# Optimization experiments

Hardware: AMD Instinct MI355X
Metric: run time of the kernel (lower is better)

The kernel has to match this reference:

```python
import jax, jax.numpy as jnp
import numpy as np

S, B, D = 2048, 2, 1024
NH, DH, DI = 16, 64, 4096


def setup_inputs() -> dict:
    key = jax.random.key(0)
    ks = jax.random.split(key, 12)
    init_qkv = 1.0 / np.sqrt(D)
    init_out = 1.0 / np.sqrt(NH * DH)
    stdm = 1.0 / np.sqrt(D)
    stdi = 1.0 / np.sqrt(DI)

    def u(k, shape, lo, hi):
        return jax.random.uniform(k, shape, jnp.float32, lo, hi)

    inp = {}
    inp["dec_inp"] = jax.random.normal(ks[0], (S, B, D), jnp.float32)
    # causal mask: True = masked (future key j > query i); shape [q, k, batch]
    causal = jnp.triu(jnp.ones((S, S), bool), k=1)
    inp["attn_mask"] = jnp.broadcast_to(causal[:, :, None], (S, S, B))
    inp["query_mean"] = u(ks[1], (NH * DH, D), -init_qkv, init_qkv)
    inp["key_mean"] = u(ks[2], (NH * DH, D), -init_qkv, init_qkv)
    inp["value_mean"] = u(ks[3], (NH * DH, D), -init_qkv, init_qkv)
    inp["query_std"] = u(ks[4], (NH * DH, D), 2 * np.log(init_qkv), np.log(init_qkv))
    inp["key_std"] = u(ks[5], (NH * DH, D), 2 * np.log(init_qkv), np.log(init_qkv))
    inp["value_std"] = u(ks[6], (NH * DH, D), 2 * np.log(init_qkv), np.log(init_qkv))
    inp["output_mean"] = u(ks[7], (D, NH * DH), -init_out, init_out)
    inp["output_std"] = u(ks[8], (D, NH * DH), 2 * np.log(init_out), np.log(init_out))
    inp["ln1_gamma"] = jnp.ones((D,), jnp.float32)
    inp["ln1_beta"] = jnp.zeros((D,), jnp.float32)
    inp["w1_mean"] = u(ks[9], (DI, D), -stdm, stdm)
    inp["w2_mean"] = u(ks[10], (D, DI), -stdi, stdi)
    inp["w1_std"] = u(ks[11], (DI, D), 2 * np.log(stdm), np.log(stdm))
    inp["w2_std"] = u(jax.random.fold_in(key, 99), (D, DI), 2 * np.log(stdi), np.log(stdi))
    inp["ln2_gamma"] = jnp.ones((D,), jnp.float32)
    inp["ln2_beta"] = jnp.zeros((D,), jnp.float32)
    return inp


def _layer_norm(x, g, b, eps=1e-5):
    mu = jnp.mean(x, -1, keepdims=True)
    var = jnp.mean((x - mu) ** 2, -1, keepdims=True)
    return g * (x - mu) * jax.lax.rsqrt(var + eps) + b


def _kl(theta_mean, theta_std):
    return jnp.mean(theta_mean ** 2 - 2.0 * theta_std + jnp.exp(2.0 * theta_std)) / 2.0


def reference(dec_inp, attn_mask, query_mean, key_mean, value_mean, query_std,
              key_std, value_std, output_mean, output_std, ln1_gamma, ln1_beta,
              w1_mean, w2_mean, w1_std, w2_std, ln2_gamma, ln2_beta):
    scale = 1.0 / (DH ** 0.5)
    # QKV projections (eval mode: no Bayesian weight sampling, diffs are 0)
    head_q = jnp.einsum('ibd,hd->ibh', dec_inp, query_mean).reshape(S, B, NH, DH)
    head_k = jnp.einsum('ibd,hd->ibh', dec_inp, key_mean).reshape(S, B, NH, DH)
    head_v = jnp.einsum('ibd,hd->ibh', dec_inp, value_mean).reshape(S, B, NH, DH)
    attn_score = jnp.einsum('ibnd,jbnd->ijbn', head_q, head_k) * scale
    attn_score = jnp.where(attn_mask[:, :, :, None], -jnp.inf, attn_score)
    attn_prob = jax.nn.softmax(attn_score, axis=1)  # softmax over key dim j
    attn_vec = jnp.einsum('ijbn,jbnd->ibnd', attn_prob, head_v).reshape(S, B, NH * DH)
    # NOTE: the original code (bug-faithfully) projects with value_mean, not output_mean
    attn_out = jnp.einsum('ibh,dh->ibd', attn_vec, value_mean)
    h = _layer_norm(dec_inp + attn_out, ln1_gamma, ln1_beta)
    attn_kl = _kl(
        jnp.concatenate([query_mean, key_mean, value_mean, output_mean.T], -1),
        jnp.concatenate([query_std, key_std, value_std, output_std.T], -1))
    # Bayesian positionwise FF (no activation in BayesPositionwiseFF)
    l1 = jnp.einsum('ibd,fd->ibf', h, w1_mean)
    l2 = jnp.einsum('ibf,df->ibd', l1, w2_mean)
    out = _layer_norm(h + l2, ln2_gamma, ln2_beta)
    ff_kl = _kl(jnp.concatenate([w1_mean, w2_mean.T], -1),
                jnp.concatenate([w1_std, w2_std.T], -1))
    return out, attn_kl + ff_kl
```

## Files before the change

kernel.cpp:

```cpp
#include <hip/hip_runtime.h>

#define S_LEN  2048
#define BATCH  2
#define DMODEL 1024
#define NHEADS 16
#define DHEAD  64
#define DFF    4096
#define MROWS  (S_LEN*BATCH)
#define QKVN   3072

typedef __attribute__((ext_vector_type(8))) short bf16x8;
typedef __attribute__((ext_vector_type(4))) float f32x4;
typedef __attribute__((ext_vector_type(4))) short s16x4;

#define NEG_BIG (-3.0e38f)
#define SCALE_LOG2 (0.125f * 1.4426950408889634f)

__device__ __forceinline__ short f2bf(float f){
  unsigned u = __float_as_uint(f);
  u += 0x7fffu + ((u >> 16) & 1u);
  return (short)(u >> 16);
}

__device__ __forceinline__ void gload16(const void* gptr, void* lptr){
  __builtin_amdgcn_global_load_lds(
      (const __attribute__((address_space(1))) unsigned int*)gptr,
      (__attribute__((address_space(3))) unsigned int*)lptr,
      16, 0, 0);
}

__global__ __launch_bounds__(256) void cast_kernel(const float* __restrict__ in,
                                                   short* __restrict__ out, int n){
  int i = (blockIdx.x * 256 + threadIdx.x) * 4;
  if (i >= n) return;
  f32x4 v = *(const f32x4*)(in + i);
  s16x4 o;
  o[0] = f2bf(v[0]); o[1] = f2bf(v[1]); o[2] = f2bf(v[2]); o[3] = f2bf(v[3]);
  *(s16x4*)(out + i) = o;
}

__global__ __launch_bounds__(256) void cast_kl_kernel(const float* __restrict__ mean,
                                                      const float* __restrict__ stdv,
                                                      short* __restrict__ outb,
                                                      int n, double* acc){
  __shared__ double red[4];
  double local = 0.0;
  const int stride = gridDim.x * 1024;
  for (int i = (blockIdx.x * 256 + threadIdx.x) * 4; i < n; i += stride){
    f32x4 m = *(const f32x4*)(mean + i);
    f32x4 sv = *(const f32x4*)(stdv + i);
    if (outb){
      s16x4 o;
      o[0] = f2bf(m[0]); o[1] = f2bf(m[1]); o[2] = f2bf(m[2]); o[3] = f2bf(m[3]);
      *(s16x4*)(outb + i) = o;
    }
    for (int e = 0; e < 4; e++)
      local += (double)(m[e] * m[e]) - 2.0 * (double)sv[e] + (double)expf(2.f * sv[e]);
  }
  for (int msk = 1; msk < 64; msk <<= 1) local += __shfl_xor(local, msk, 64);
  const int t = threadIdx.x;
  if ((t & 63) == 0) red[t >> 6] = local;
  __syncthreads();
  if (t == 0) atomicAdd(acc, red[0] + red[1] + red[2] + red[3]);
}

__global__ void kl_final(const double* acc, float* out){
  out[0] = (float)(acc[0] / 8388608.0 + acc[1] / 16777216.0);
}

template<int BN>
__global__ __launch_bounds__(512) void gemm_bt(const short* __restrict__ A,
                                               const short* __restrict__ Bt,
                                               float* __restrict__ Cf,
                                               short* __restrict__ Cb,
                                               int M, int N, int K, int nbx){
  __shared__ short As[2][128][32];
  __shared__ short Bs[2][BN][32];
  constexpr int NB = BN / 32;
  const int t = threadIdx.x;
  const int lane = t & 63, w = t >> 6;
  const int q8 = (int)gridDim.x >> 3;
  const int sid = ((int)blockIdx.x & 7) * q8 + ((int)blockIdx.x >> 3);
  const int bx = sid % nbx, by = sid / nbx;
  const int m0 = by * 128, n0 = bx * BN;
  const int wm = (w & 3) * 32, wn = (w >> 2) * (BN / 2);
  const int lr = lane & 15, lg = lane >> 4;

  f32x4 acc[2][NB] = {};

  const short* Ap = A  + (size_t)(m0 + (t >> 2)) * K + (t & 3) * 8;
  const short* Bp = Bt + (size_t)(n0 + ((t & (BN * 4 - 1)) >> 2)) * K + (t & 3) * 8;
  char* ldsA0 = (char*)As + w * 1024;
  char* ldsB0 = (char*)Bs + (w & (NB * 2 - 1)) * 1024;
  constexpr int BSTRIDE = BN * 64;

  gload16(Ap, ldsA0);
  if (BN == 128 || t < 256) gload16(Bp, ldsB0);
  asm volatile("s_waitcnt vmcnt(0)" ::: "memory");
  __builtin_amdgcn_s_barrier();
  asm volatile("" ::: "memory");

  int cur = 0;
  for (int k0 = 0; k0 < K; k0 += 32){
    if (k0 + 32 < K){
      gload16(Ap + k0 + 32, ldsA0 + (cur ^ 1) * 8192);
      if (BN == 128 || t < 256) gload16(Bp + k0 + 32, ldsB0 + (cur ^ 1) * BSTRIDE);
    }
    bf16x8 a0 = *(const bf16x8*)&As[cur][wm      + lr][lg * 8];
    bf16x8 a1 = *(const bf16x8*)&As[cur][wm + 16 + lr][lg * 8];
    bf16x8 bfr[NB];
    for (int ni = 0; ni < NB; ni++)
      bfr[ni] = *(const bf16x8*)&Bs[cur][wn + ni * 16 + lr][lg * 8];
    for (int ni = 0; ni < NB; ni++){
      acc[0][ni] = __builtin_amdgcn_mfma_f32_16x16x32_bf16(a0, bfr[ni], acc[0][ni], 0, 0, 0);
      acc[1][ni] = __builtin_amdgcn_mfma_f32_16x16x32_bf16(a1, bfr[ni], acc[1][ni], 0, 0, 0);
    }
    asm volatile("s_waitcnt vmcnt(0)" ::: "memory");
    __builtin_amdgcn_s_barrier();
    asm volatile("" ::: "memory");
    cur ^= 1;
  }

  for (int mi = 0; mi < 2; mi++){
    for (int ni = 0; ni < NB; ni++){
      int row = m0 + wm + mi * 16 + lg * 4;
      int col = n0 + wn + ni * 16 + lr;
      for (int r = 0; r < 4; r++){
        float v = acc[mi][ni][r];
        if (Cf) Cf[(size_t)(row + r) * N + col] = v;
        if (Cb) Cb[(size_t)(row + r) * N + col] = f2bf(v);
      }
    }
  }
}

__global__ __launch_bounds__(256) void attn_kernel(const short* __restrict__ QKV,
                                                   short* __restrict__ AV){
  __shared__ short Ks[64][64];
  __shared__ short Vst[64][64];
  __shared__ short Pt[4][16][64];
  const int t = threadIdx.x, lane = t & 63, w = t >> 6;
  const int hb = blockIdx.y;
  const int b = hb >> 4, n = hb & 15;
  const int lr = lane & 15, lg = lane >> 4;

  for (int half = 0; half < 2; half++){
    const int qt = half ? (31 - (int)blockIdx.x) : (int)blockIdx.x;
    const int q0w = qt * 64 + w * 16;

    bf16x8 aq[2];
    {
      const short* qp = QKV + ((size_t)(q0w + lr) * BATCH + b) * QKVN + n * DHEAD + lg * 8;
      aq[0] = *(const bf16x8*)(qp);
      aq[1] = *(const bf16x8*)(qp + 32);
    }

    f32x4 acc[4] = {};
    float m_run = NEG_BIG, l_run = 0.f;

    for (int jt = 0; jt <= qt; jt++){
      const int j0 = jt * 64;
      __syncthreads();
      {
        int j = t >> 2, u0 = (t & 3) * 2;
        const short* kp = QKV + ((size_t)(j0 + j) * BATCH + b) * QKVN + DMODEL + n * DHEAD + u0 * 8;
        *(bf16x8*)&Ks[j][(u0 ^ (j & 7)) * 8]       = *(const bf16x8*)(kp);
        *(bf16x8*)&Ks[j][((u0 + 1) ^ (j & 7)) * 8] = *(const bf16x8*)(kp + 8);
        int jv = t & 63, dq = (t >> 6) * 16;
        const short* vp = QKV + ((size_t)(j0 + jv) * BATCH + b) * QKVN + 2 * DMODEL + n * DHEAD + dq;
        bf16x8 v0 = *(const bf16x8*)(vp);
        bf16x8 v1 = *(const bf16x8*)(vp + 8);
        int uj = jv >> 3, jl = jv & 7;
        for (int e = 0; e < 8; e++){
          int sc = (((uj ^ e) << 3) | jl);
          Vst[dq + e][sc]     = v0[e];
          Vst[dq + 8 + e][sc] = v1[e];
        }
      }
      __syncthreads();

      f32x4 s[4];
      __builtin_amdgcn_s_setprio(1);
      for (int nf = 0; nf < 4; nf++){
        f32x4 z = {};
        for (int kk = 0; kk < 2; kk++){
          bf16x8 bk = *(const bf16x8*)&Ks[nf * 16 + lr][((kk * 4 + lg) ^ (lr & 7)) * 8];
          z = __builtin_amdgcn_mfma_f32_16x16x32_bf16(bk, aq[kk], z, 0, 0, 0);
        }
        s[nf] = z;
      }
      __builtin_amdgcn_s_setprio(0);

      for (int nf = 0; nf < 4; nf++)
        for (int r = 0; r < 4; r++) s[nf][r] *= SCALE_LOG2;

      if (jt == qt){
        int qg = q0w + lr;
        for (int nf = 0; nf < 4; nf++)
          for (int r = 0; r < 4; r++)
            if (j0 + nf * 16 + lg * 4 + r > qg) s[nf][r] = NEG_BIG;
      }

      float mx = NEG_BIG;
      for (int nf = 0; nf < 4; nf++){
        float a0 = fmaxf(s[nf][0], s[nf][1]);
        float a1 = fmaxf(s[nf][2], s[nf][3]);
        mx = fmaxf(mx, fmaxf(a0, a1));
      }
      mx = fmaxf(mx, __shfl_xor(mx, 16, 64));
      mx = fmaxf(mx, __shfl_xor(mx, 32, 64));
      float mn = fmaxf(m_run, mx);
      float corr = __builtin_exp2f(m_run - mn);
      m_run = mn;

      float rs = 0.f;
      for (int nf = 0; nf < 4; nf++)
        for (int r = 0; r < 4; r++){
          float p = __builtin_exp2f(s[nf][r] - mn);
          s[nf][r] = p;
          rs += p;
        }
      rs += __shfl_xor(rs, 16, 64);
      rs += __shfl_xor(rs, 32, 64);
      l_run = l_run * corr + rs;

      char* prow = (char*)&Pt[w][lr][0];
      for (int nf = 0; nf < 4; nf++){
        unsigned u0 = __float_as_uint(s[nf][0]);
        unsigned u1 = __float_as_uint(s[nf][1]);
        unsigned u2 = __float_as_uint(s[nf][2]);
        unsigned u3 = __float_as_uint(s[nf][3]);
        uint2 val;
        val.x = (u0 >> 16) | (u1 & 0xffff0000u);
        val.y = (u2 >> 16) | (u3 & 0xffff0000u);
        int off = ((((nf * 2) + (lg >> 1)) ^ (lr & 7)) << 4) + ((lg & 1) << 3);
        *(uint2*)(prow + off) = val;
      }

      float cb[4];
      for (int r = 0; r < 4; r++) cb[r] = __shfl(corr, lg * 4 + r, 64);
      for (int df = 0; df < 4; df++)
        for (int r = 0; r < 4; r++) acc[df][r] *= cb[r];

      __builtin_amdgcn_s_setprio(1);
      for (int kk = 0; kk < 2; kk++){
        bf16x8 pa = *(const bf16x8*)(prow + ((((kk * 4) + lg) ^ (lr & 7)) << 4));
        for (int df = 0; df < 4; df++){
          bf16x8 bv = *(const bf16x8*)&Vst[df * 16 + lr][((kk * 4 + lg) ^ (lr & 7)) * 8];
          acc[df] = __builtin_amdgcn_mfma_f32_16x16x32_bf16(pa, bv, acc[df], 0, 0, 0);
        }
      }
      __builtin_amdgcn_s_setprio(0);
    }

    float lb[4];
    for (int r = 0; r < 4; r++) lb[r] = __shfl(l_run, lg * 4 + r, 64);
    for (int df = 0; df < 4; df++){
      for (int r = 0; r < 4; r++){
        int i_glob = q0w + lg * 4 + r;
        AV[((size_t)i_glob * BATCH + b) * DMODEL + n * DHEAD + df * 16 + lr] =
            f2bf(acc[df][r] / lb[r]);
      }
    }
    __syncthreads();
  }
}

__global__ __launch_bounds__(256) void ln_kernel(const float* __restrict__ xa,
                                                 const float* __restrict__ xb,
                                                 const float* __restrict__ gamma,
                                                 const float* __restrict__ beta,
                                                 float* __restrict__ outF,
                                                 short* __restrict__ outB){
  __shared__ float red[4];
  const int row = blockIdx.x, t = threadIdx.x;
  const size_t base = (size_t)row * DMODEL + t * 4;
  f32x4 a  = *(const f32x4*)(xa + base);
  f32x4 bb = *(const f32x4*)(xb + base);
  f32x4 x;
  for (int e = 0; e < 4; e++) x[e] = a[e] + bb[e];
  float sum = x[0] + x[1] + x[2] + x[3];
  for (int m = 1; m < 64; m <<= 1) sum += __shfl_xor(sum, m, 64);
  if ((t & 63) == 0) red[t >> 6] = sum;
  __syncthreads();
  float mu = (red[0] + red[1] + red[2] + red[3]) * (1.f / DMODEL);
  float sq = 0.f;
  for (int e = 0; e < 4; e++){ float d = x[e] - mu; sq += d * d; }
  for (int m = 1; m < 64; m <<= 1) sq += __shfl_xor(sq, m, 64);
  __syncthreads();
  if ((t & 63) == 0) red[t >> 6] = sq;
  __syncthreads();
  float var = (red[0] + red[1] + red[2] + red[3]) * (1.f / DMODEL);
  float rstd = rsqrtf(var + 1e-5f);
  f32x4 g  = *(const f32x4*)(gamma + t * 4);
  f32x4 be = *(const f32x4*)(beta + t * 4);
  for (int e = 0; e < 4; e++){
    float y = g[e] * (x[e] - mu) * rstd + be[e];
    if (outF) outF[base + e] = y;
    if (outB) outB[base + e] = f2bf(y);
  }
}

extern "C" void kernel_launch(void* const* d_in, const int* in_sizes, int n_in,
                              void* d_out, int out_size, void* d_ws, size_t ws_size,
                              hipStream_t stream){
  (void)in_sizes; (void)n_in; (void)out_size; (void)ws_size;
  const float* dec = (const float*)d_in[0];
  const float* qm  = (const float*)d_in[2];
  const float* km  = (const float*)d_in[3];
  const float* vm  = (const float*)d_in[4];
  const float* qs  = (const float*)d_in[5];
  const float* ks  = (const float*)d_in[6];
  const float* vs  = (const float*)d_in[7];
  const float* om  = (const float*)d_in[8];
  const float* os_ = (const float*)d_in[9];
  const float* g1  = (const float*)d_in[10];
  const float* b1  = (const float*)d_in[11];
  const float* w1m = (const float*)d_in[12];
  const float* w2m = (const float*)d_in[13];
  const float* w1s = (const float*)d_in[14];
  const float* w2s = (const float*)d_in[15];
  const float* g2  = (const float*)d_in[16];
  const float* b2  = (const float*)d_in[17];
  float* out = (float*)d_out;

  char* ws = (char*)d_ws;
  size_t off = 0;
  auto alloc = [&](size_t bytes) -> char* {
    char* p = ws + off;
    off += (bytes + 255) & ~(size_t)255;
    return p;
  };
  short* Xb   = (short*)alloc((size_t)MROWS * DMODEL * 2);
  short* Wqkv = (short*)alloc((size_t)QKVN * DMODEL * 2);
  short* W1   = (short*)alloc((size_t)DFF * DMODEL * 2);
  short* W2   = (short*)alloc((size_t)DMODEL * DFF * 2);
  short* Wv   = Wqkv + (size_t)2 * DMODEL * DMODEL;
  short* QKVb = (short*)alloc((size_t)MROWS * QKVN * 2);
  short* AVb  = (short*)alloc((size_t)MROWS * DMODEL * 2);
  float* tmpF = (float*)alloc((size_t)MROWS * DMODEL * 4);
  float* hF   = (float*)alloc((size_t)MROWS * DMODEL * 4);
  double* acc = (double*)alloc(256);
  short* L1 = QKVb;

  hipMemsetAsync(acc, 0, 16, stream);

  cast_kernel<<<MROWS * DMODEL / 1024, 256, 0, stream>>>(dec, Xb, MROWS * DMODEL);
  cast_kl_kernel<<<1024, 256, 0, stream>>>(qm, qs, Wqkv, DMODEL * DMODEL, acc);
  cast_kl_kernel<<<1024, 256, 0, stream>>>(km, ks, Wqkv + (size_t)DMODEL * DMODEL, DMODEL * DMODEL, acc);
  cast_kl_kernel<<<1024, 256, 0, stream>>>(vm, vs, Wqkv + (size_t)2 * DMODEL * DMODEL, DMODEL * DMODEL, acc);
  cast_kl_kernel<<<1024, 256, 0, stream>>>(om, os_, nullptr, DMODEL * DMODEL, acc);
  cast_kl_kernel<<<1024, 256, 0, stream>>>(w1m, w1s, W1, DFF * DMODEL, acc + 1);
  cast_kl_kernel<<<1024, 256, 0, stream>>>(w2m, w2s, W2, DMODEL * DFF, acc + 1);

  gemm_bt<128><<<(QKVN / 128) * (MROWS / 128), 512, 0, stream>>>(Xb, Wqkv, nullptr, QKVb, MROWS, QKVN, DMODEL, QKVN / 128);

  attn_kernel<<<dim3(16, BATCH * NHEADS), 256, 0, stream>>>(QKVb, AVb);

  gemm_bt<64><<<(DMODEL / 64) * (MROWS / 128), 512, 0, stream>>>(AVb, Wv, tmpF, nullptr, MROWS, DMODEL, DMODEL, DMODEL / 64);

  ln_kernel<<<MROWS, 256, 0, stream>>>(dec, tmpF, g1, b1, hF, Xb);

  gemm_bt<128><<<(DFF / 128) * (MROWS / 128), 512, 0, stream>>>(Xb, W1, nullptr, L1, MROWS, DFF, DMODEL, DFF / 128);
  gemm_bt<64><<<(DMODEL / 64) * (MROWS / 128), 512, 0, stream>>>(L1, W2, tmpF, nullptr, MROWS, DMODEL, DFF, DMODEL / 64);

  ln_kernel<<<MROWS, 256, 0, stream>>>(hF, tmpF, g2, b2, out, nullptr);

  kl_final<<<1, 1, 0, stream>>>(acc, out + (size_t)MROWS * DMODEL);
}
```

Measured before the change: 523.4 us.

## Deepen GEMM LDS pipeline to four stages and restructure attention grid with lazy rescale

The GEMM moves from double to quad LDS buffering. It keeps three K-tiles in flight, uses partial vmcnt waits, and raises MFMA priority, so global load latency overlaps with compute. The attention kernel stops pairing two query tiles per block and launches one block per query tile, doubling the grid. It applies the FlashAttention-style lazy max update, rescaling only when the row max grows by more than a threshold, and folds the scale into an fma. The costs are 4x LDS in the GEMM, which may lower occupancy, and workload imbalance across causal attention blocks that the old pairing had evened out.

```diff
diff --git a/kernel.cpp b/kernel.cpp
--- a/kernel.cpp
+++ b/kernel.cpp
@@ -74,9 +74,10 @@
                                                float* __restrict__ Cf,
                                                short* __restrict__ Cb,
                                                int M, int N, int K, int nbx){
-  __shared__ short As[2][128][32];
-  __shared__ short Bs[2][BN][32];
+  __shared__ short As[4][128][32];
+  __shared__ short Bs[4][BN][32];
   constexpr int NB = BN / 32;
+  constexpr int BSTRIDE = BN * 64;
   const int t = threadIdx.x;
   const int lane = t & 63, w = t >> 6;
   const int q8 = (int)gridDim.x >> 3;
@@ -85,6 +86,8 @@
   const int m0 = by * 128, n0 = bx * BN;
   const int wm = (w & 3) * 32, wn = (w >> 2) * (BN / 2);
   const int lr = lane & 15, lg = lane >> 4;
+  const bool doB = (BN == 128) || (t < 256);
+  const bool twoLoads = (BN == 128) || (w < 4);
 
   f32x4 acc[2][NB] = {};
 
@@ -92,33 +95,45 @@
   const short* Bp = Bt + (size_t)(n0 + ((t & (BN * 4 - 1)) >> 2)) * K + (t & 3) * 8;
   char* ldsA0 = (char*)As + w * 1024;
   char* ldsB0 = (char*)Bs + (w & (NB * 2 - 1)) * 1024;
-  constexpr int BSTRIDE = BN * 64;
-
-  gload16(Ap, ldsA0);
-  if (BN == 128 || t < 256) gload16(Bp, ldsB0);
-  asm volatile("s_waitcnt vmcnt(0)" ::: "memory");
-  __builtin_amdgcn_s_barrier();
-  asm volatile("" ::: "memory");
-
-  int cur = 0;
-  for (int k0 = 0; k0 < K; k0 += 32){
-    if (k0 + 32 < K){
-      gload16(Ap + k0 + 32, ldsA0 + (cur ^ 1) * 8192);
-      if (BN == 128 || t < 256) gload16(Bp + k0 + 32, ldsB0 + (cur ^ 1) * BSTRIDE);
-    }
+
+  const int nk = K / 32;
+  for (int p = 0; p < 3; p++){
+    gload16(Ap + p * 32, ldsA0 + p * 8192);
+    if (doB) gload16(Bp + p * 32, ldsB0 + p * BSTRIDE);
+  }
+
+  for (int kt = 0; kt < nk; kt++){
+    const int rem = nk - 1 - kt;
+    if (twoLoads){
+      if (rem >= 2)      asm volatile("s_waitcnt vmcnt(4)" ::: "memory");
+      else if (rem == 1) asm volatile("s_waitcnt vmcnt(2)" ::: "memory");
+      else               asm volatile("s_waitcnt vmcnt(0)" ::: "memory");
+    } else {
+      if (rem >= 2)      asm volatile("s_waitcnt vmcnt(2)" ::: "memory");
+      else if (rem == 1) asm volatile("s_waitcnt vmcnt(1)" ::: "memory");
+      else               asm volatile("s_waitcnt vmcnt(0)" ::: "memory");
+    }
+    __builtin_amdgcn_s_barrier();
+    asm volatile("" ::: "memory");
+
+    const int nxt = kt + 3;
+    if (nxt < nk){
+      gload16(Ap + nxt * 32, ldsA0 + (nxt & 3) * 8192);
+      if (doB) gload16(Bp + nxt * 32, ldsB0 + (nxt & 3) * BSTRIDE);
+    }
+
+    const int cur = kt & 3;
     bf16x8 a0 = *(const bf16x8*)&As[cur][wm      + lr][lg * 8];
     bf16x8 a1 = *(const bf16x8*)&As[cur][wm + 16 + lr][lg * 8];
     bf16x8 bfr[NB];
     for (int ni = 0; ni < NB; ni++)
       bfr[ni] = *(const bf16x8*)&Bs[cur][wn + ni * 16 + lr][lg * 8];
+    __builtin_amdgcn_s_setprio(1);
     for (int ni = 0; ni < NB; ni++){
       acc[0][ni] = __builtin_amdgcn_mfma_f32_16x16x32_bf16(a0, bfr[ni], acc[0][ni], 0, 0, 0);
       acc[1][ni] = __builtin_amdgcn_mfma_f32_16x16x32_bf16(a1, bfr[ni], acc[1][ni], 0, 0, 0);
     }
-    asm volatile("s_waitcnt vmcnt(0)" ::: "memory");
-    __builtin_amdgcn_s_barrier();
-    asm volatile("" ::: "memory");
-    cur ^= 1;
+    __builtin_amdgcn_s_setprio(0);
   }
 
   for (int mi = 0; mi < 2; mi++){
@@ -144,125 +159,123 @@
   const int b = hb >> 4, n = hb & 15;
   const int lr = lane & 15, lg = lane >> 4;
 
-  for (int half = 0; half < 2; half++){
-    const int qt = half ? (31 - (int)blockIdx.x) : (int)blockIdx.x;
-    const int q0w = qt * 64 + w * 16;
-
-    bf16x8 aq[2];
+  const int qt = 31 - (int)blockIdx.x;
+  const int q0w = qt * 64 + w * 16;
+
+  bf16x8 aq[2];
+  {
+    const short* qp = QKV + ((size_t)(q0w + lr) * BATCH + b) * QKVN + n * DHEAD + lg * 8;
+    aq[0] = *(const bf16x8*)(qp);
+    aq[1] = *(const bf16x8*)(qp + 32);
+  }
+
+  f32x4 acc[4] = {};
+  float m_run = NEG_BIG, l_run = 0.f;
+
+  for (int jt = 0; jt <= qt; jt++){
+    const int j0 = jt * 64;
+    __syncthreads();
     {
-      const short* qp = QKV + ((size_t)(q0w + lr) * BATCH + b) * QKVN + n * DHEAD + lg * 8;
-      aq[0] = *(const bf16x8*)(qp);
-      aq[1] = *(const bf16x8*)(qp + 32);
-    }
-
-    f32x4 acc[4] = {};
-    float m_run = NEG_BIG, l_run = 0.f;
-
-    for (int jt = 0; jt <= qt; jt++){
-      const int j0 = jt * 64;
-      __syncthreads();
-      {
-        int j = t >> 2, u0 = (t & 3) * 2;
-        const short* kp = QKV + ((size_t)(j0 + j) * BATCH + b) * QKVN + DMODEL + n * DHEAD + u0 * 8;
-        *(bf16x8*)&Ks[j][(u0 ^ (j & 7)) * 8]       = *(const bf16x8*)(kp);
-        *(bf16x8*)&Ks[j][((u0 + 1) ^ (j & 7)) * 8] = *(const bf16x8*)(kp + 8);
-        int jv = t & 63, dq = (t >> 6) * 16;
-        const short* vp = QKV + ((size_t)(j0 + jv) * BATCH + b) * QKVN + 2 * DMODEL + n * DHEAD + dq;
-        bf16x8 v0 = *(const bf16x8*)(vp);
-        bf16x8 v1 = *(const bf16x8*)(vp + 8);
-        int uj = jv >> 3, jl = jv & 7;
-        for (int e = 0; e < 8; e++){
-          int sc = (((uj ^ e) << 3) | jl);
-          Vst[dq + e][sc]     = v0[e];
-          Vst[dq + 8 + e][sc] = v1[e];
-        }
-      }
-      __syncthreads();
-
-      f32x4 s[4];
-      __builtin_amdgcn_s_setprio(1);
-      for (int nf = 0; nf < 4; nf++){
-        f32x4 z = {};
-        for (int kk = 0; kk < 2; kk++){
-          bf16x8 bk = *(const bf16x8*)&Ks[nf * 16 + lr][((kk * 4 + lg) ^ (lr & 7)) * 8];
-          z = __builtin_amdgcn_mfma_f32_16x16x32_bf16(bk, aq[kk], z, 0, 0, 0);
-        }
-        s[nf] = z;
-      }
-      __builtin_amdgcn_s_setprio(0);
-
+      int j = t >> 2, u0 = (t & 3) * 2;
+      const short* kp = QKV + ((size_t)(j0 + j) * BATCH + b) * QKVN + DMODEL + n * DHEAD + u0 * 8;
+      *(bf16x8*)&Ks[j][(u0 ^ (j & 7)) * 8]       = *(const bf16x8*)(kp);
+      *(bf16x8*)&Ks[j][((u0 + 1) ^ (j & 7)) * 8] = *(const bf16x8*)(kp + 8);
+      int jv = t & 63, dq = (t >> 6) * 16;
+      const short* vp = QKV + ((size_t)(j0 + jv) * BATCH + b) * QKVN + 2 * DMODEL + n * DHEAD + dq;
+      bf16x8 v0 = *(const bf16x8*)(vp);
+      bf16x8 v1 = *(const bf16x8*)(vp + 8);
+      int uj = jv >> 3, jl = jv & 7;
+      for (int e = 0; e < 8; e++){
+        int sc = (((uj ^ e) << 3) | jl);
+        Vst[dq + e][sc]     = v0[e];
+        Vst[dq + 8 + e][sc] = v1[e];
+      }
+    }
+    __syncthreads();
+
+    f32x4 s[4];
+    __builtin_amdgcn_s_setprio(1);
+    for (int nf = 0; nf < 4; nf++){
+      f32x4 z = {};
+      for (int kk = 0; kk < 2; kk++){
+        bf16x8 bk = *(const bf16x8*)&Ks[nf * 16 + lr][((kk * 4 + lg) ^ (lr & 7)) * 8];
+        z = __builtin_amdgcn_mfma_f32_16x16x32_bf16(bk, aq[kk], z, 0, 0, 0);
+      }
+      s[nf] = z;
+    }
+    __builtin_amdgcn_s_setprio(0);
+
+    if (jt == qt){
+      int qg = q0w + lr;
       for (int nf = 0; nf < 4; nf++)
-        for (int r = 0; r < 4; r++) s[nf][r] *= SCALE_LOG2;
-
-      if (jt == qt){
-        int qg = q0w + lr;
-        for (int nf = 0; nf < 4; nf++)
-          for (int r = 0; r < 4; r++)
-            if (j0 + nf * 16 + lg * 4 + r > qg) s[nf][r] = NEG_BIG;
-      }
-
-      float mx = NEG_BIG;
-      for (int nf = 0; nf < 4; nf++){
-        float a0 = fmaxf(s[nf][0], s[nf][1]);
-        float a1 = fmaxf(s[nf][2], s[nf][3]);
-        mx = fmaxf(mx, fmaxf(a0, a1));
-      }
-      mx = fmaxf(mx, __shfl_xor(mx, 16, 64));
-      mx = fmaxf(mx, __shfl_xor(mx, 32, 64));
-      float mn = fmaxf(m_run, mx);
+        for (int r = 0; r < 4; r++)
+          if (j0 + nf * 16 + lg * 4 + r > qg) s[nf][r] = NEG_BIG;
+    }
+
+    float mx = NEG_BIG;
+    for (int nf = 0; nf < 4; nf++){
+      float a0 = fmaxf(s[nf][0], s[nf][1]);
+      float a1 = fmaxf(s[nf][2], s[nf][3]);
+      mx = fmaxf(mx, fmaxf(a0, a1));
+    }
+    mx = fmaxf(mx, __shfl_xor(mx, 16, 64));
+    mx = fmaxf(mx, __shfl_xor(mx, 32, 64));
+    float mxs = mx * SCALE_LOG2;
+
+    if (__any(mxs > m_run + 8.f)){
+      float mn = fmaxf(m_run, mxs);
       float corr = __builtin_exp2f(m_run - mn);
       m_run = mn;
-
-      float rs = 0.f;
-      for (int nf = 0; nf < 4; nf++)
-        for (int r = 0; r < 4; r++){
-          float p = __builtin_exp2f(s[nf][r] - mn);
-          s[nf][r] = p;
-          rs += p;
-        }
-      rs += __shfl_xor(rs, 16, 64);
-      rs += __shfl_xor(rs, 32, 64);
-      l_run = l_run * corr + rs;
-
-      char* prow = (char*)&Pt[w][lr][0];
-      for (int nf = 0; nf < 4; nf++){
-        unsigned u0 = __float_as_uint(s[nf][0]);
-        unsigned u1 = __float_as_uint(s[nf][1]);
-        unsigned u2 = __float_as_uint(s[nf][2]);
-        unsigned u3 = __float_as_uint(s[nf][3]);
-        uint2 val;
-        val.x = (u0 >> 16) | (u1 & 0xffff0000u);
-        val.y = (u2 >> 16) | (u3 & 0xffff0000u);
-        int off = ((((nf * 2) + (lg >> 1)) ^ (lr & 7)) << 4) + ((lg & 1) << 3);
-        *(uint2*)(prow + off) = val;
-      }
-
+      l_run *= corr;
       float cb[4];
       for (int r = 0; r < 4; r++) cb[r] = __shfl(corr, lg * 4 + r, 64);
       for (int df = 0; df < 4; df++)
         for (int r = 0; r < 4; r++) acc[df][r] *= cb[r];
-
-      __builtin_amdgcn_s_setprio(1);
-      for (int kk = 0; kk < 2; kk++){
-        bf16x8 pa = *(const bf16x8*)(prow + ((((kk * 4) + lg) ^ (lr & 7)) << 4));
-        for (int df = 0; df < 4; df++){
-          bf16x8 bv = *(const bf16x8*)&Vst[df * 16 + lr][((kk * 4 + lg) ^ (lr & 7)) * 8];
-          acc[df] = __builtin_amdgcn_mfma_f32_16x16x32_bf16(pa, bv, acc[df], 0, 0, 0);
-        }
-      }
-      __builtin_amdgcn_s_setprio(0);
-    }
-
-    float lb[4];
-    for (int r = 0; r < 4; r++) lb[r] = __shfl(l_run, lg * 4 + r, 64);
-    for (int df = 0; df < 4; df++){
+    }
+
+    float rs = 0.f;
+    for (int nf = 0; nf < 4; nf++)
       for (int r = 0; r < 4; r++){
-        int i_glob = q0w + lg * 4 + r;
-        AV[((size_t)i_glob * BATCH + b) * DMODEL + n * DHEAD + df * 16 + lr] =
-            f2bf(acc[df][r] / lb[r]);
-      }
-    }
-    __syncthreads();
+        float p = __builtin_exp2f(fmaf(s[nf][r], SCALE_LOG2, -m_run));
+        s[nf][r] = p;
+        rs += p;
+      }
+    rs += __shfl_xor(rs, 16, 64);
+    rs += __shfl_xor(rs, 32, 64);
+    l_run += rs;
+
+    char* prow = (char*)&Pt[w][lr][0];
+    for (int nf = 0; nf < 4; nf++){
+      unsigned u0 = __float_as_uint(s[nf][0]);
+      unsigned u1 = __float_as_uint(s[nf][1]);
+      unsigned u2 = __float_as_uint(s[nf][2]);
+      unsigned u3 = __float_as_uint(s[nf][3]);
+      uint2 val;
+      val.x = (u0 >> 16) | (u1 & 0xffff0000u);
+      val.y = (u2 >> 16) | (u3 & 0xffff0000u);
+      int off = ((((nf * 2) + (lg >> 1)) ^ (lr & 7)) << 4) + ((lg & 1) << 3);
+      *(uint2*)(prow + off) = val;
+    }
+
+    __builtin_amdgcn_s_setprio(1);
+    for (int kk = 0; kk < 2; kk++){
+      bf16x8 pa = *(const bf16x8*)(prow + ((((kk * 4) + lg) ^ (lr & 7)) << 4));
+      for (int df = 0; df < 4; df++){
+        bf16x8 bv = *(const bf16x8*)&Vst[df * 16 + lr][((kk * 4 + lg) ^ (lr & 7)) * 8];
+        acc[df] = __builtin_amdgcn_mfma_f32_16x16x32_bf16(pa, bv, acc[df], 0, 0, 0);
+      }
+    }
+    __builtin_amdgcn_s_setprio(0);
+  }
+
+  float lb[4];
+  for (int r = 0; r < 4; r++) lb[r] = __shfl(l_run, lg * 4 + r, 64);
+  for (int df = 0; df < 4; df++){
+    for (int r = 0; r < 4; r++){
+      int i_glob = q0w + lg * 4 + r;
+      AV[((size_t)i_glob * BATCH + b) * DMODEL + n * DHEAD + df * 16 + lr] =
+          f2bf(acc[df][r] / lb[r]);
+    }
   }
 }
 
@@ -355,7 +368,7 @@
 
   gemm_bt<128><<<(QKVN / 128) * (MROWS / 128), 512, 0, stream>>>(Xb, Wqkv, nullptr, QKVb, MROWS, QKVN, DMODEL, QKVN / 128);
 
-  attn_kernel<<<dim3(16, BATCH * NHEADS), 256, 0, stream>>>(QKVb, AVb);
+  attn_kernel<<<dim3(32, BATCH * NHEADS), 256, 0, stream>>>(QKVb, AVb);
 
   gemm_bt<64><<<(DMODEL / 64) * (MROWS / 128), 512, 0, stream>>>(AVb, Wv, tmpF, nullptr, MROWS, DMODEL, DMODEL, DMODEL / 64);
 
```

New measurement: 565.9 us. 1.08x slower.
